# Kernel optimization log

Measured on AMD Instinct MI355X. Metric: run time of the kernel, lower is better.

Reference implementation:

```python
import jax, jax.numpy as jnp
import numpy as np

NUM_ORI = 4
VM_R, VM_RG = 10.0, 15.0
B_INH, G_INH = 1.5, 1.0
VM_W, VM_W2 = 0.1, 0.4
VM_WG, VM_W2G = 0.2, 0.4
BORDER_K = 11   # int(10*1.1)=11, already odd
GROUP_K = 23    # int(15*1.5)=22 -> +1 to make odd


def create_von_mises(size, r0, theta0, centered, w, w2):
    x = np.arange(size) - size / 2
    y = -(np.arange(size) - size / 2)
    X, Y = np.meshgrid(x, y)
    if centered:
        X = X + r0 * np.cos(theta0)
        Y = Y + r0 * np.sin(theta0)
    r = np.sqrt(X ** 2 + Y ** 2)
    th = np.arctan2(Y, X)
    # np.i0 == scipy.special.iv(0, .) for real args (I0 is even)
    return np.exp(r0 * w * np.cos(th - theta0)) / np.i0(w2 * (r - r0))


def make_filters():
    borders, groups = [], []
    for ori in np.arange(0.0, 180.0, 180.0 / NUM_ORI):
        a = ori * np.pi / 180.0
        b = (ori + 180.0) * np.pi / 180.0
        borders.append(create_von_mises(BORDER_K, VM_R, a, True, VM_W, VM_W2))
        borders.append(create_von_mises(BORDER_K, VM_R, b, True, VM_W, VM_W2))
        g1 = create_von_mises(GROUP_K, VM_RG, a, False, VM_W, VM_W2)
        g2 = create_von_mises(GROUP_K, VM_RG, b, False, VM_WG, VM_W2G)
        groups += [g1, g1, g2, g2]
    # only border filters are normalized to [-1, 1] in the original code
    borders = [f / (f.max() / 2.0) - 1.0 for f in borders]
    Wb = np.stack(borders)[:, None].astype(np.float32)   # [2*O, 1, 11, 11]
    Wg = np.stack(groups)[:, None].astype(np.float32)    # [4*O, 1, 23, 23]
    return jnp.asarray(Wb), jnp.asarray(Wg)


def setup_inputs() -> dict:
    key = jax.random.key(0)
    inp = jax.random.uniform(key, (4, 2, 512, 512), dtype=jnp.float32)
    Wb, Wg = make_filters()
    return {"inp": inp, "W_border": Wb, "W_group": Wg}


def _conv(x, w, pad, groups):
    return jax.lax.conv_general_dilated(
        x, w, (1, 1), [(pad, pad), (pad, pad)],
        dimension_numbers=("NCHW", "OIHW", "NCHW"),
        feature_group_count=groups)


def _spike(v):
    # LIF with tau_mem=0.01, zero initial v_mem, single step: alpha=exp(-1/tau)~0,
    # so v_mem = input; spike when v_mem >= threshold (1.0).
    return (v >= 1.0).astype(v.dtype)


def reference(inp, W_border, W_group):
    B, _, H, W = inp.shape
    pad_b = (BORDER_K - 1) // 2
    pad_g = (GROUP_K - 1) // 2
    # border ownership: conv each polarity with the 8 von-Mises filters + LIF
    pos = _spike(_conv(inp[:, 0:1], W_border, pad_b, 1))  # [B, 2*O, H, W]
    neg = _spike(_conv(inp[:, 1:2], W_border, pad_b, 1))
    vmap_ = inp.sum(1)[:, None]                           # [B, 1, H, W]
    pe, po = pos[:, 0::2], pos[:, 1::2]   # even=ori, odd=opposite ori
    ne, no = neg[:, 0::2], neg[:, 1::2]
    b13 = _spike(vmap_ * (pe - no * B_INH)) + _spike(vmap_ * (ne - po * B_INH))
    b24 = _spike(vmap_ * (po - ne * B_INH)) + _spike(vmap_ * (no - pe * B_INH))
    # winner-take-all over orientations
    diff = b13 - b24                                      # [B, O, H, W]
    tp = jnp.abs(diff)
    wta = jax.lax.stop_gradient(
        (tp == tp.max(axis=1, keepdims=True)).astype(inp.dtype))
    b1p = _spike(wta * diff)
    b1n = _spike(-(wta * diff))
    # channel order is ori-major: [t1_o, t2_o, t3_o, t4_o] per orientation
    border = jnp.stack(
        [b1p * b13, b1p * b24 * G_INH, b1n * b24, b1n * b13 * G_INH],
        axis=2).reshape(B, 4 * NUM_ORI, H, W)
    g = _spike(_conv(border, W_group, pad_g, 4 * NUM_ORI))
    g = g.reshape(B, NUM_ORI, 4, H, W)
    return (_spike(g[:, :, 0] - g[:, :, 1])
            + _spike(g[:, :, 2] - g[:, :, 3])).sum(1)     # [B, H, W]
```

## Files before the change

### kernel.cpp

```cpp
#include <hip/hip_runtime.h>

#define HH 512
#define WW 512
#define NB 4

typedef float v2f __attribute__((ext_vector_type(2)));

#define WG3_ELEMS 88320

__global__ __launch_bounds__(256) void prep_kernel(
    const float* __restrict__ Wg, float* __restrict__ Wg3)
{
    const int e = blockIdx.x * 256 + threadIdx.x;
    if (e >= WG3_ELEMS) return;
    const int d  = e & 7;
    const int r  = e >> 3;
    const int kx = r % 23;
    const int r2 = r / 23;
    const int t  = r2 % 30;
    const int c  = r2 / 30;
    const int ky = t - d;
    Wg3[e] = (ky >= 0 && ky < 23) ? Wg[c * 529 + ky * 23 + kx] : 0.f;
}

#define K1 11
#define PAD1 5
#define T1X 32
#define T1Y 32
#define IN1 42
#define S1B 44

__global__ __launch_bounds__(256, 4) void stage1_kernel(
    const float* __restrict__ inp, const float* __restrict__ Wb,
    unsigned char* __restrict__ border)
{
    __shared__ __align__(16) float s0[IN1 * S1B];
    __shared__ __align__(16) float s1[IN1 * S1B];

    const int b   = blockIdx.z;
    const int tx0 = blockIdx.x * T1X;
    const int ty0 = blockIdx.y * T1Y;
    const float* in0 = inp + ((size_t)b * 2 + 0) * (HH * WW);
    const float* in1 = inp + ((size_t)b * 2 + 1) * (HH * WW);

    for (int i = threadIdx.x; i < IN1 * IN1; i += 256) {
        int iy = i / IN1, ix = i - iy * IN1;
        int gy = ty0 + iy - PAD1, gx = tx0 + ix - PAD1;
        bool ok = (gy >= 0) & (gy < HH) & (gx >= 0) & (gx < WW);
        int idx = gy * WW + gx;
        s0[iy * S1B + ix] = ok ? in0[idx] : 0.f;
        s1[iy * S1B + ix] = ok ? in1[idx] : 0.f;
    }
    __syncthreads();

    const int lx  = threadIdx.x & 7;
    const int ly  = threadIdx.x >> 3;
    const int px0 = lx * 4;
    const int py  = ly;

    float accP[8][4], accN[8][4];
    #pragma unroll
    for (int c = 0; c < 8; c++)
        #pragma unroll
        for (int p = 0; p < 4; p++) { accP[c][p] = 0.f; accN[c][p] = 0.f; }

    #pragma unroll 1
    for (int ky = 0; ky < K1; ky++) {
        float a0[14], a1[14];
        const float2* r0 = (const float2*)&s0[(py + ky) * S1B + px0];
        const float2* r1 = (const float2*)&s1[(py + ky) * S1B + px0];
        #pragma unroll
        for (int r = 0; r < 7; r++) {
            *(float2*)&a0[2 * r] = r0[r];
            *(float2*)&a1[2 * r] = r1[r];
        }
        #pragma unroll
        for (int c = 0; c < 8; c++) {
            #pragma unroll
            for (int kx = 0; kx < K1; kx++) {
                const float wv = Wb[c * 121 + ky * 11 + kx];
                #pragma unroll
                for (int p = 0; p < 4; p++) {
                    accP[c][p] = fmaf(a0[kx + p], wv, accP[c][p]);
                    accN[c][p] = fmaf(a1[kx + p], wv, accN[c][p]);
                }
            }
        }
    }

    const int gy  = ty0 + py;
    const int gxb = tx0 + px0;

    float vm[4];
    #pragma unroll
    for (int p = 0; p < 4; p++)
        vm[p] = s0[(py + PAD1) * S1B + px0 + PAD1 + p]
              + s1[(py + PAD1) * S1B + px0 + PAD1 + p];

    float b13[4][4], b24[4][4];
    #pragma unroll
    for (int o = 0; o < 4; o++) {
        #pragma unroll
        for (int p = 0; p < 4; p++) {
            float pe = (accP[2 * o    ][p] >= 1.f) ? 1.f : 0.f;
            float po = (accP[2 * o + 1][p] >= 1.f) ? 1.f : 0.f;
            float ne = (accN[2 * o    ][p] >= 1.f) ? 1.f : 0.f;
            float no = (accN[2 * o + 1][p] >= 1.f) ? 1.f : 0.f;
            float sa = (vm[p] * (pe - 1.5f * no) >= 1.f) ? 1.f : 0.f;
            float sb = (vm[p] * (ne - 1.5f * po) >= 1.f) ? 1.f : 0.f;
            b13[o][p] = sa + sb;
            float sc = (vm[p] * (po - 1.5f * ne) >= 1.f) ? 1.f : 0.f;
            float sd = (vm[p] * (no - 1.5f * pe) >= 1.f) ? 1.f : 0.f;
            b24[o][p] = sc + sd;
        }
    }
    float mxp[4];
    #pragma unroll
    for (int p = 0; p < 4; p++) {
        float m = 0.f;
        #pragma unroll
        for (int o = 0; o < 4; o++) m = fmaxf(m, fabsf(b13[o][p] - b24[o][p]));
        mxp[p] = m;
    }
    #pragma unroll
    for (int o = 0; o < 4; o++) {
        unsigned w0 = 0, w1 = 0, w2 = 0, w3 = 0;
        #pragma unroll
        for (int p = 0; p < 4; p++) {
            float d   = b13[o][p] - b24[o][p];
            float wta = (fabsf(d) == mxp[p]) ? 1.f : 0.f;
            float b1p = (wta * d >= 1.f)    ? 1.f : 0.f;
            float b1n = (-(wta * d) >= 1.f) ? 1.f : 0.f;
            w0 |= (unsigned)(unsigned char)(b1p * b13[o][p]) << (8 * p);
            w1 |= (unsigned)(unsigned char)(b1p * b24[o][p]) << (8 * p);
            w2 |= (unsigned)(unsigned char)(b1n * b24[o][p]) << (8 * p);
            w3 |= (unsigned)(unsigned char)(b1n * b13[o][p]) << (8 * p);
        }
        size_t base = (((size_t)b * 16 + 4 * o) * HH + gy) * WW + gxb;
        *(unsigned*)&border[base]                       = w0;
        *(unsigned*)&border[base + (size_t)HH * WW]     = w1;
        *(unsigned*)&border[base + (size_t)2 * HH * WW] = w2;
        *(unsigned*)&border[base + (size_t)3 * HH * WW] = w3;
    }
}

#define K2 23
#define PAD2 11
#define T2X 32
#define T2Y 512
#define SROW 18
#define R2 534

__device__ __forceinline__ float ubyte_f(unsigned dw, int byi) {
    return (float)((dw >> (8 * byi)) & 0xffu);
}

__device__ __forceinline__ void s2_load(const unsigned* __restrict__ tile,
                                        int trow, int lx, unsigned d[8])
{
    const uint2* tp2 = (const uint2*)&tile[trow * SROW + 2 * lx];
    #pragma unroll
    for (int r2 = 0; r2 < 4; r2++) {
        uint2 v = tp2[r2];
        d[2 * r2] = v.x; d[2 * r2 + 1] = v.y;
    }
}

__global__ __launch_bounds__(256, 4) void stage2_kernel(
    const unsigned char* __restrict__ border, const float* __restrict__ Wg3,
    unsigned char* __restrict__ gsp)
{
    __shared__ unsigned tile[R2 * SROW];

    const int z   = blockIdx.z;
    const int b   = z >> 4;
    const int c   = z & 15;
    const int tx0 = blockIdx.x * T2X;
    const unsigned char* bp = border + ((size_t)b * 16 + c) * (HH * WW);

    for (int i = threadIdx.x; i < R2 * 16; i += 256) {
        int iy = i >> 4, cc = i & 15;
        int gy  = iy - PAD2;
        int gx0 = tx0 - 12 + 4 * cc;
        unsigned u = 0;
        if (((unsigned)gy < HH) & ((unsigned)gx0 < WW))
            u = *(const unsigned*)(bp + (size_t)gy * WW + gx0);
        tile[iy * SROW + cc] = u;
    }
    __syncthreads();

    const int lx = threadIdx.x & 3;
    const int ly = threadIdx.x >> 2;
    const int px = lx * 8;
    const int py = ly * 8;

    v2f acc2[4][8];
    #pragma unroll
    for (int d2 = 0; d2 < 4; d2++)
        #pragma unroll
        for (int p = 0; p < 8; p++) acc2[d2][p] = (v2f){0.f, 0.f};

    const float* wc3 = Wg3 + (size_t)c * (30 * 184);

    unsigned dc[8];
    s2_load(tile, py + 0, lx, dc);

    #pragma unroll 1
    for (int t = 0; t < 30; t++) {
        float cv[30];
        #pragma unroll
        for (int j = 0; j < 30; j++) cv[j] = ubyte_f(dc[(j + 1) >> 2], (j + 1) & 3);
        if (t < 29) s2_load(tile, py + t + 1, lx, dc);

        const v2f* wt = (const v2f*)(wc3 + t * 184);
        #pragma unroll
        for (int kx = 0; kx < K2; kx++) {
            #pragma unroll
            for (int p = 0; p < 8; p++) {
                const float cs = cv[p + kx];
                const v2f cb = {cs, cs};
                #pragma unroll
                for (int d2 = 0; d2 < 4; d2++)
                    acc2[d2][p] = __builtin_elementwise_fma(cb, wt[kx * 4 + d2],
                                                            acc2[d2][p]);
            }
        }
    }

    const int ox = tx0 + px;
    unsigned char* gp = gsp + ((size_t)b * 16 + c) * (HH * WW);
    #pragma unroll
    for (int dy = 0; dy < 8; dy++) {
        const int oy = py + dy;
        unsigned lo = 0, hi = 0;
        #pragma unroll
        for (int p = 0; p < 4; p++) {
            float av = (dy & 1) ? acc2[dy >> 1][p].y : acc2[dy >> 1][p].x;
            lo |= (av >= 1.f ? 1u : 0u) << (8 * p);
        }
        #pragma unroll
        for (int p = 0; p < 4; p++) {
            float av = (dy & 1) ? acc2[dy >> 1][p + 4].y : acc2[dy >> 1][p + 4].x;
            hi |= (av >= 1.f ? 1u : 0u) << (8 * p);
        }
        uint2 v; v.x = lo; v.y = hi;
        *(uint2*)&gp[(size_t)oy * WW + ox] = v;
    }
}

__global__ __launch_bounds__(256) void combine_kernel(
    const unsigned char* __restrict__ gsp, float* __restrict__ out)
{
    const int idx = blockIdx.x * 256 + threadIdx.x;
    const int b = idx >> 16;
    const int r = idx & 65535;
    const unsigned* g = (const unsigned*)gsp;
    const int pb = b * 16;
    unsigned s = 0;
    #pragma unroll
    for (int o = 0; o < 4; o++) {
        unsigned g0 = g[(size_t)(pb + 4 * o + 0) * 65536 + r];
        unsigned g1 = g[(size_t)(pb + 4 * o + 1) * 65536 + r];
        unsigned g2 = g[(size_t)(pb + 4 * o + 2) * 65536 + r];
        unsigned g3 = g[(size_t)(pb + 4 * o + 3) * 65536 + r];
        s += ((g0 & ~g1) & 0x01010101u) + ((g2 & ~g3) & 0x01010101u);
    }
    float4 f;
    f.x = (float)(s & 255u);
    f.y = (float)((s >> 8) & 255u);
    f.z = (float)((s >> 16) & 255u);
    f.w = (float)(s >> 24);
    ((float4*)out)[idx] = f;
}

extern "C" void kernel_launch(void* const* d_in, const int* in_sizes, int n_in,
                              void* d_out, int out_size, void* d_ws, size_t ws_size,
                              hipStream_t stream)
{
    const float* inp = (const float*)d_in[0];
    const float* Wb  = (const float*)d_in[1];
    const float* Wg  = (const float*)d_in[2];
    unsigned char* border = (unsigned char*)d_ws;
    unsigned char* gsp    = border + (size_t)NB * 16 * HH * WW;
    float* out = (float*)d_out;

    float* Wg3 = (float*)((char*)d_out + (2u << 20));

    dim3 blk(256);
    prep_kernel<<<dim3((WG3_ELEMS + 255) / 256), blk, 0, stream>>>(Wg, Wg3);
    dim3 g1(WW / T1X, HH / T1Y, NB);
    stage1_kernel<<<g1, blk, 0, stream>>>(inp, Wb, border);
    dim3 g2(WW / T2X, 1, NB * 16);
    stage2_kernel<<<g2, blk, 0, stream>>>(border, Wg3, gsp);
    dim3 g3((NB * HH * WW / 4) / 256);
    combine_kernel<<<g3, blk, 0, stream>>>(gsp, out);
}
```

Baseline: 307.0 us.

## Restructure group conv to pack adjacent pixels in v2f and drop weight prep kernel

Removes the prep kernel that expanded the group weights into a row-shifted, zero-padded layout, and reads the raw 23x23 weights directly in stage2. Each thread now covers 4 rows by 8 pixels instead of 8 by 8, and the packed v2f FMA lanes hold two horizontally adjacent pixels built from even/odd shifted byte vectors, rather than two output rows. The grid is split in half along Y to double block count. This avoids the extra launch and the zero-padded multiplies, at the cost of scalar weight loads behind per-row bounds checks and more halo reloading per output.

```diff
diff --git a/kernel.cpp b/kernel.cpp
--- a/kernel.cpp
+++ b/kernel.cpp
@@ -5,23 +5,6 @@
 #define NB 4
 
 typedef float v2f __attribute__((ext_vector_type(2)));
-
-#define WG3_ELEMS 88320
-
-__global__ __launch_bounds__(256) void prep_kernel(
-    const float* __restrict__ Wg, float* __restrict__ Wg3)
-{
-    const int e = blockIdx.x * 256 + threadIdx.x;
-    if (e >= WG3_ELEMS) return;
-    const int d  = e & 7;
-    const int r  = e >> 3;
-    const int kx = r % 23;
-    const int r2 = r / 23;
-    const int t  = r2 % 30;
-    const int c  = r2 / 30;
-    const int ky = t - d;
-    Wg3[e] = (ky >= 0 && ky < 23) ? Wg[c * 529 + ky * 23 + kx] : 0.f;
-}
 
 #define K1 11
 #define PAD1 5
@@ -147,9 +130,9 @@
 #define K2 23
 #define PAD2 11
 #define T2X 32
-#define T2Y 512
+#define T2Y 256
 #define SROW 18
-#define R2 534
+#define R2 278
 
 __device__ __forceinline__ float ubyte_f(unsigned dw, int byi) {
     return (float)((dw >> (8 * byi)) & 0xffu);
@@ -167,7 +150,7 @@
 }
 
 __global__ __launch_bounds__(256, 4) void stage2_kernel(
-    const unsigned char* __restrict__ border, const float* __restrict__ Wg3,
+    const unsigned char* __restrict__ border, const float* __restrict__ Wg,
     unsigned char* __restrict__ gsp)
 {
     __shared__ unsigned tile[R2 * SROW];
@@ -176,11 +159,12 @@
     const int b   = z >> 4;
     const int c   = z & 15;
     const int tx0 = blockIdx.x * T2X;
+    const int ty0 = blockIdx.y * T2Y;
     const unsigned char* bp = border + ((size_t)b * 16 + c) * (HH * WW);
 
     for (int i = threadIdx.x; i < R2 * 16; i += 256) {
         int iy = i >> 4, cc = i & 15;
-        int gy  = iy - PAD2;
+        int gy  = ty0 - PAD2 + iy;
         int gx0 = tx0 - 12 + 4 * cc;
         unsigned u = 0;
         if (((unsigned)gy < HH) & ((unsigned)gx0 < WW))
@@ -192,37 +176,48 @@
     const int lx = threadIdx.x & 3;
     const int ly = threadIdx.x >> 2;
     const int px = lx * 8;
-    const int py = ly * 8;
-
-    v2f acc2[4][8];
-    #pragma unroll
-    for (int d2 = 0; d2 < 4; d2++)
-        #pragma unroll
-        for (int p = 0; p < 8; p++) acc2[d2][p] = (v2f){0.f, 0.f};
-
-    const float* wc3 = Wg3 + (size_t)c * (30 * 184);
+    const int py = ly * 4;
+
+    v2f acc2[4][4];
+    #pragma unroll
+    for (int dy = 0; dy < 4; dy++)
+        #pragma unroll
+        for (int i = 0; i < 4; i++) acc2[dy][i] = (v2f){0.f, 0.f};
+
+    const float* wc = Wg + c * (K2 * K2);
 
     unsigned dc[8];
     s2_load(tile, py + 0, lx, dc);
 
     #pragma unroll 1
-    for (int t = 0; t < 30; t++) {
-        float cv[30];
-        #pragma unroll
-        for (int j = 0; j < 30; j++) cv[j] = ubyte_f(dc[(j + 1) >> 2], (j + 1) & 3);
-        if (t < 29) s2_load(tile, py + t + 1, lx, dc);
-
-        const v2f* wt = (const v2f*)(wc3 + t * 184);
-        #pragma unroll
-        for (int kx = 0; kx < K2; kx++) {
-            #pragma unroll
-            for (int p = 0; p < 8; p++) {
-                const float cs = cv[p + kx];
-                const v2f cb = {cs, cs};
+    for (int t = 0; t < 26; t++) {
+        v2f aE[15], aO[15];
+        #pragma unroll
+        for (int e = 0; e < 15; e++)
+            aE[e] = (v2f){ubyte_f(dc[(2*e)   >> 2], (2*e)   & 3),
+                          ubyte_f(dc[(2*e+1) >> 2], (2*e+1) & 3)};
+        #pragma unroll
+        for (int o = 0; o < 15; o++)
+            aO[o] = (v2f){ubyte_f(dc[(2*o+1) >> 2], (2*o+1) & 3),
+                          ubyte_f(dc[(2*o+2) >> 2], (2*o+2) & 3)};
+        if (t < 25) s2_load(tile, py + t + 1, lx, dc);
+
+        #pragma unroll
+        for (int dy = 0; dy < 4; dy++) {
+            const int ky = t - dy;
+            if (ky >= 0 && ky < K2) {
+                const float* wr = wc + ky * K2;
                 #pragma unroll
-                for (int d2 = 0; d2 < 4; d2++)
-                    acc2[d2][p] = __builtin_elementwise_fma(cb, wt[kx * 4 + d2],
-                                                            acc2[d2][p]);
+                for (int kx = 0; kx < K2; kx++) {
+                    const float wv = wr[kx];
+                    const v2f wb = (v2f){wv, wv};
+                    #pragma unroll
+                    for (int i = 0; i < 4; i++) {
+                        const v2f op = (kx & 1) ? aE[i + (kx + 1) / 2]
+                                                : aO[i + kx / 2];
+                        acc2[dy][i] = __builtin_elementwise_fma(op, wb, acc2[dy][i]);
+                    }
+                }
             }
         }
     }
@@ -230,18 +225,18 @@
     const int ox = tx0 + px;
     unsigned char* gp = gsp + ((size_t)b * 16 + c) * (HH * WW);
     #pragma unroll
-    for (int dy = 0; dy < 8; dy++) {
-        const int oy = py + dy;
+    for (int dy = 0; dy < 4; dy++) {
+        const int oy = ty0 + py + dy;
         unsigned lo = 0, hi = 0;
         #pragma unroll
-        for (int p = 0; p < 4; p++) {
-            float av = (dy & 1) ? acc2[dy >> 1][p].y : acc2[dy >> 1][p].x;
-            lo |= (av >= 1.f ? 1u : 0u) << (8 * p);
-        }
-        #pragma unroll
-        for (int p = 0; p < 4; p++) {
-            float av = (dy & 1) ? acc2[dy >> 1][p + 4].y : acc2[dy >> 1][p + 4].x;
-            hi |= (av >= 1.f ? 1u : 0u) << (8 * p);
+        for (int i = 0; i < 2; i++) {
+            lo |= (acc2[dy][i].x >= 1.f ? 1u : 0u) << (16 * i);
+            lo |= (acc2[dy][i].y >= 1.f ? 1u : 0u) << (16 * i + 8);
+        }
+        #pragma unroll
+        for (int i = 0; i < 2; i++) {
+            hi |= (acc2[dy][i + 2].x >= 1.f ? 1u : 0u) << (16 * i);
+            hi |= (acc2[dy][i + 2].y >= 1.f ? 1u : 0u) << (16 * i + 8);
         }
         uint2 v; v.x = lo; v.y = hi;
         *(uint2*)&gp[(size_t)oy * WW + ox] = v;
@@ -284,14 +279,11 @@
     unsigned char* gsp    = border + (size_t)NB * 16 * HH * WW;
     float* out = (float*)d_out;
 
-    float* Wg3 = (float*)((char*)d_out + (2u << 20));
-
     dim3 blk(256);
-    prep_kernel<<<dim3((WG3_ELEMS + 255) / 256), blk, 0, stream>>>(Wg, Wg3);
     dim3 g1(WW / T1X, HH / T1Y, NB);
     stage1_kernel<<<g1, blk, 0, stream>>>(inp, Wb, border);
-    dim3 g2(WW / T2X, 1, NB * 16);
-    stage2_kernel<<<g2, blk, 0, stream>>>(border, Wg3, gsp);
+    dim3 g2(WW / T2X, HH / T2Y, NB * 16);
+    stage2_kernel<<<g2, blk, 0, stream>>>(border, Wg, gsp);
     dim3 g3((NB * HH * WW / 4) / 256);
     combine_kernel<<<g3, blk, 0, stream>>>(gsp, out);
 }
```

New measurement: 277.1 us. 9.8% less time.
